# Optimization experiments

Measured on AMD Instinct MI355X. Metric: run time of the kernel, lower is better.

The kernel has to match this reference:

```python
import jax, jax.numpy as jnp
import numpy as np

D_MODEL = 1024
D_FF = 4096
N_EXPERTS = 8
TOP_K = 2
TEMP = 0.7
B, L = 4, 2048


def setup_inputs() -> dict:
    key = jax.random.key(0)
    ks = jax.random.split(key, 6)
    s = 0.02  # init scale
    return {
        "x": jax.random.normal(ks[0], (B, L, D_MODEL), jnp.float32),
        "Wr": jax.random.normal(ks[1], (D_MODEL, N_EXPERTS), jnp.float32) * s,
        "br": jnp.zeros((N_EXPERTS,), jnp.float32),
        "W1": jax.random.normal(ks[2], (N_EXPERTS, D_MODEL, D_FF), jnp.float32) * s,
        "b1": jnp.zeros((N_EXPERTS, D_FF), jnp.float32),
        "W2": jax.random.normal(ks[3], (N_EXPERTS, D_FF, D_MODEL), jnp.float32) * s,
        "b2": jnp.zeros((N_EXPERTS, D_MODEL), jnp.float32),
    }


def reference(x, Wr, br, W1, b1, W2, b2):
    # Eval-mode MoE: no router jitter, dropout is identity.
    Bb, Ll, Dd = x.shape
    E = Wr.shape[1]
    xf = x.reshape(-1, Dd)                              # [T, D]
    T = xf.shape[0]

    logits = xf @ Wr + br                               # [T, E]
    probs = jax.nn.softmax(logits / TEMP, axis=-1)      # [T, E]
    top_w, top_i = jax.lax.top_k(probs, TOP_K)          # [T, K]
    top_w = top_w / (jnp.sum(top_w, axis=-1, keepdims=True) + 1e-6)

    # Per-token per-expert combine weight (zero for non-selected experts).
    cw = jnp.zeros((T, E), xf.dtype).at[jnp.arange(T)[:, None], top_i].add(top_w)

    out = jnp.zeros_like(xf)
    for e in range(E):  # small fixed expert loop
        h = jax.nn.silu(xf @ W1[e] + b1[e])             # [T, d_ff]
        out = out + cw[:, e:e + 1] * (h @ W2[e] + b2[e])

    # Load-balance aux loss.
    counts = jnp.zeros((E,), xf.dtype).at[top_i.reshape(-1)].add(1.0)
    f_i = counts / T
    P_i = probs.mean(axis=0)
    aux = E * jnp.sum(f_i * P_i)
    return out.reshape(Bb, Ll, Dd), aux[None]
```

## Files before the change

### kernel.cpp

```cpp
#include <hip/hip_runtime.h>

#define DM     1024
#define DFF    4096
#define NE     8
#define TT     8192
#define CAP    8192
#define TILE   128
#define RTOK   32
#define MAXROWS 17408

typedef __bf16 bf16x8 __attribute__((ext_vector_type(8)));
typedef float  f32x4  __attribute__((ext_vector_type(4)));
typedef unsigned short u16;
typedef unsigned int   u32;

__device__ __forceinline__ u16 f2bf(float f) {
    u32 u = __builtin_bit_cast(u32, f);
    u += 0x7fffu + ((u >> 16) & 1u);
    return (u16)(u >> 16);
}

__device__ __forceinline__ void gload_lds16(const void* g, void* l) {
    __builtin_amdgcn_global_load_lds(
        (const __attribute__((address_space(1))) void*)g,
        (__attribute__((address_space(3))) void*)l,
        16, 0, 0);
}

__global__ __launch_bounds__(256) void router_k(
    const float* __restrict__ x, const float* __restrict__ Wr, const float* __restrict__ br,
    int* __restrict__ expert_count, float* __restrict__ prob_sum,
    int* __restrict__ list_token, float* __restrict__ list_w,
    int* __restrict__ tok_e, int* __restrict__ tok_q, float* __restrict__ tok_w)
{
    __shared__ float wrT[NE][DM];
    __shared__ float ps[NE];
    __shared__ int   lcount[NE];
    __shared__ int   lbase[NE];
    __shared__ int   lexp[RTOK * 2];
    __shared__ float lw[RTOK * 2];
    __shared__ int   lslot[RTOK * 2];

    int tid = threadIdx.x;
    if (tid < NE) { ps[tid] = 0.f; lcount[tid] = 0; }
#pragma unroll
    for (int it = 0; it < 8; ++it) {
        int f = tid * 4 + it * 1024;
        float4 v = *reinterpret_cast<const float4*>(Wr + f);
        int e0 = f & 7, k = f >> 3;
        wrT[e0][k] = v.x; wrT[e0 + 1][k] = v.y; wrT[e0 + 2][k] = v.z; wrT[e0 + 3][k] = v.w;
    }
    __syncthreads();

    int w = tid >> 6, l = tid & 63;
    for (int j = 0; j < RTOK / 4; ++j) {
        int ti = w * (RTOK / 4) + j;
        int token = blockIdx.x * RTOK + ti;
        const float* xr = x + (size_t)token * DM;
        float acc[NE];
#pragma unroll
        for (int e = 0; e < NE; ++e) acc[e] = 0.f;
#pragma unroll
        for (int i = 0; i < 4; ++i) {
            float4 xv = *reinterpret_cast<const float4*>(xr + i * 256 + l * 4);
#pragma unroll
            for (int e = 0; e < NE; ++e) {
                float4 wv = *reinterpret_cast<const float4*>(&wrT[e][i * 256 + l * 4]);
                acc[e] += xv.x * wv.x + xv.y * wv.y + xv.z * wv.z + xv.w * wv.w;
            }
        }
#pragma unroll
        for (int off = 32; off >= 1; off >>= 1) {
#pragma unroll
            for (int e = 0; e < NE; ++e) acc[e] += __shfl_xor(acc[e], off);
        }
        if (l == 0) {
            float li[NE], m = -1e30f;
#pragma unroll
            for (int e = 0; e < NE; ++e) { li[e] = (acc[e] + br[e]) * (1.0f / 0.7f); m = fmaxf(m, li[e]); }
            float p[NE], s = 0.f;
#pragma unroll
            for (int e = 0; e < NE; ++e) { p[e] = __expf(li[e] - m); s += p[e]; }
            float inv = 1.f / s;
#pragma unroll
            for (int e = 0; e < NE; ++e) { p[e] *= inv; atomicAdd(&ps[e], p[e]); }
            float v1 = -1.f, v2 = -1.f; int e1 = 0, e2 = 0;
#pragma unroll
            for (int e = 0; e < NE; ++e) {
                float pe = p[e];
                if (pe > v1)      { v2 = v1; e2 = e1; v1 = pe; e1 = e; }
                else if (pe > v2) { v2 = pe; e2 = e; }
            }
            float denom = v1 + v2 + 1e-6f;
            lexp[2 * ti]     = e1; lw[2 * ti]     = v1 / denom; lslot[2 * ti]     = atomicAdd(&lcount[e1], 1);
            lexp[2 * ti + 1] = e2; lw[2 * ti + 1] = v2 / denom; lslot[2 * ti + 1] = atomicAdd(&lcount[e2], 1);
        }
    }
    __syncthreads();
    if (tid < NE) {
        lbase[tid] = atomicAdd(&expert_count[tid], lcount[tid]);
        atomicAdd(&prob_sum[tid], ps[tid]);
    }
    __syncthreads();
    if (tid < RTOK * 2) {
        int e = lexp[tid];
        int q = lbase[e] + lslot[tid];
        int token = blockIdx.x * RTOK + (tid >> 1);
        list_token[e * CAP + q] = token;
        list_w[e * CAP + q] = lw[tid];
        int slot = token * 2 + (tid & 1);
        tok_e[slot] = e; tok_q[slot] = q; tok_w[slot] = lw[tid];
    }
}

__global__ void scan_aux_k(const int* __restrict__ expert_count, const float* __restrict__ prob_sum,
                           int* __restrict__ padded_count, int* __restrict__ poffsets,
                           float* __restrict__ aux_out)
{
    if (threadIdx.x == 0 && blockIdx.x == 0) {
        int off = 0; float aux = 0.f;
        for (int e = 0; e < NE; ++e) {
            int c = expert_count[e];
            int pc = (c + TILE - 1) / TILE * TILE;
            poffsets[e] = off; padded_count[e] = pc; off += pc;
            aux += ((float)c / (float)TT) * (prob_sum[e] / (float)TT);
        }
        aux_out[0] = aux * (float)NE;
    }
}

__global__ __launch_bounds__(256) void gather_k(
    const float* __restrict__ x, const int* __restrict__ list_token,
    const int* __restrict__ expert_count, const int* __restrict__ padded_count,
    const int* __restrict__ poffsets, u16* __restrict__ Xg)
{
    int e = blockIdx.y;
    int p0 = blockIdx.x * 8;
    if (p0 >= padded_count[e]) return;
    int tid = threadIdx.x;
    int rr = tid >> 5, cl = tid & 31;
    int p = p0 + rr;
    int g = poffsets[e] + p;
    u16* dst = Xg + (size_t)g * DM;
    bool valid = p < expert_count[e];
    int tok = valid ? list_token[e * CAP + p] : 0;
    const float* src = x + (size_t)tok * DM;
#pragma unroll
    for (int i = 0; i < 4; ++i) {
        int c0 = cl * 8 + i * 256;
        uint4 v;
        if (valid) {
            float4 f0 = *reinterpret_cast<const float4*>(src + c0);
            float4 f1 = *reinterpret_cast<const float4*>(src + c0 + 4);
            v.x = f2bf(f0.x) | ((u32)f2bf(f0.y) << 16);
            v.y = f2bf(f0.z) | ((u32)f2bf(f0.w) << 16);
            v.z = f2bf(f1.x) | ((u32)f2bf(f1.y) << 16);
            v.w = f2bf(f1.z) | ((u32)f2bf(f1.w) << 16);
        } else {
            v.x = 0; v.y = 0; v.z = 0; v.w = 0;
        }
        *reinterpret_cast<uint4*>(dst + c0) = v;
    }
}

__global__ __launch_bounds__(256) void convt_k(
    const float* __restrict__ src, u16* __restrict__ dst, long base, int rs, int Ktot, long dstEStride)
{
    __shared__ float tile[64][65];
    int e = blockIdx.z;
    int k0 = blockIdx.x * 64, j0 = blockIdx.y * 64;
    const float* s = src + (size_t)e * 4194304 + base;
    int tid = threadIdx.x;
    {
        int jj = (tid & 15) * 4, kb = tid >> 4;
#pragma unroll
        for (int i = 0; i < 4; ++i) {
            int k = kb + i * 16;
            float4 v = *reinterpret_cast<const float4*>(s + (size_t)(k0 + k) * rs + j0 + jj);
            tile[k][jj] = v.x; tile[k][jj + 1] = v.y; tile[k][jj + 2] = v.z; tile[k][jj + 3] = v.w;
        }
    }
    __syncthreads();
    {
        int kk = (tid & 15) * 4, jb = tid >> 4;
        u16* d = dst + (size_t)e * dstEStride;
#pragma unroll
        for (int i = 0; i < 4; ++i) {
            int j = jb + i * 16;
            uint2 q;
            q.x = f2bf(tile[kk][j])     | ((u32)f2bf(tile[kk + 1][j]) << 16);
            q.y = f2bf(tile[kk + 2][j]) | ((u32)f2bf(tile[kk + 3][j]) << 16);
            *reinterpret_cast<uint2*>(d + (size_t)(j0 + j) * Ktot + k0 + kk) = q;
        }
    }
}

__device__ __forceinline__ void stage_tile(const u16* __restrict__ rows, long lda, int kt, char* buf) {
    int tid = threadIdx.x;
    int w = tid >> 6, l = tid & 63;
#pragma unroll
    for (int i = 0; i < 4; ++i) {
        int sbase = i * 256 + w * 64;
        int sl = sbase + l;
        int row = sl >> 3;
        int c8 = (sl & 7) ^ (row & 7);
        const u16* src = rows + (size_t)row * lda + kt * 64 + c8 * 8;
        gload_lds16(src, buf + sbase * 16);
    }
}

__device__ __forceinline__ void gemm_main(
    const u16* __restrict__ Arows, long lda,
    const u16* __restrict__ Brows, long ldb,
    int nkt, char* smem, f32x4 acc[4][4])
{
    int tid = threadIdx.x;
    int l = tid & 63, lane16 = l & 15, hi = l >> 4;
    int wm = (tid >> 6) & 1, wn = tid >> 7;

    for (int kt = 0; kt < nkt; ++kt) {
        stage_tile(Arows, lda, kt, smem);
        stage_tile(Brows, ldb, kt, smem + 16384);
        __syncthreads();
        const char* bufA = smem;
        const char* bufB = smem + 16384;
#pragma unroll
        for (int kk = 0; kk < 2; ++kk) {
            bf16x8 af[4], bb[4];
#pragma unroll
            for (int mi = 0; mi < 4; ++mi) {
                int row = wm * 64 + mi * 16 + lane16;
                int ch = (kk * 4 + hi) ^ (row & 7);
                af[mi] = *reinterpret_cast<const bf16x8*>(bufA + (row * 8 + ch) * 16);
            }
#pragma unroll
            for (int ni = 0; ni < 4; ++ni) {
                int row = wn * 64 + ni * 16 + lane16;
                int ch = (kk * 4 + hi) ^ (row & 7);
                bb[ni] = *reinterpret_cast<const bf16x8*>(bufB + (row * 8 + ch) * 16);
            }
#pragma unroll
            for (int mi = 0; mi < 4; ++mi)
#pragma unroll
                for (int ni = 0; ni < 4; ++ni)
                    acc[mi][ni] = __builtin_amdgcn_mfma_f32_16x16x32_bf16(af[mi], bb[ni], acc[mi][ni], 0, 0, 0);
        }
        __syncthreads();
    }
}

__global__ __launch_bounds__(256, 4) void gemm1_k(
    const u16* __restrict__ Xg, const u16* __restrict__ W1c, const float* __restrict__ b1,
    int ffBase, int chunkN, const int* __restrict__ padded_count, const int* __restrict__ poffsets,
    u16* __restrict__ H)
{
    __shared__ char smem[32768];
    int e = blockIdx.z, rb = blockIdx.y, cb = blockIdx.x;
    if (rb * TILE >= padded_count[e]) return;
    int row0 = poffsets[e] + rb * TILE;
    const u16* Arows = Xg + (size_t)row0 * 1024;
    const u16* Brows = W1c + (size_t)e * chunkN * 1024 + (size_t)cb * TILE * 1024;
    f32x4 acc[4][4];
#pragma unroll
    for (int i = 0; i < 4; ++i)
#pragma unroll
        for (int j = 0; j < 4; ++j) { acc[i][j][0]=0.f; acc[i][j][1]=0.f; acc[i][j][2]=0.f; acc[i][j][3]=0.f; }
    gemm_main(Arows, 1024, Brows, 1024, 16, smem, acc);

    int tid = threadIdx.x;
    int l = tid & 63, lane16 = l & 15, hi = l >> 4;
    int wm = (tid >> 6) & 1, wn = tid >> 7;
    const float* b1e = b1 + (size_t)e * DFF + ffBase;
#pragma unroll
    for (int mi = 0; mi < 4; ++mi) {
#pragma unroll
        for (int ni = 0; ni < 4; ++ni) {
            int col = cb * TILE + wn * 64 + ni * 16 + lane16;
            float bv = b1e[col];
#pragma unroll
            for (int r = 0; r < 4; ++r) {
                int grow = row0 + wm * 64 + mi * 16 + hi * 4 + r;
                float z = acc[mi][ni][r] + bv;
                float hval = z / (1.f + __expf(-z));
                H[(size_t)grow * chunkN + col] = f2bf(hval);
            }
        }
    }
}

__global__ __launch_bounds__(256, 4) void gemm2_k(
    const u16* __restrict__ Hb, const u16* __restrict__ W2c, const float* __restrict__ b2,
    int chunkK, int mode, const int* __restrict__ expert_count, const int* __restrict__ padded_count,
    const int* __restrict__ poffsets, const int* __restrict__ list_token,
    const float* __restrict__ list_w, float* __restrict__ Og, float* __restrict__ out)
{
    __shared__ char smem[32768];
    int e = blockIdx.z, rb = blockIdx.y, cb = blockIdx.x;
    if (rb * TILE >= padded_count[e]) return;
    int row0 = poffsets[e] + rb * TILE;
    const u16* Arows = Hb + (size_t)row0 * chunkK;
    const u16* Brows = W2c + (size_t)e * DM * chunkK + (size_t)cb * TILE * chunkK;
    f32x4 acc[4][4];
#pragma unroll
    for (int i = 0; i < 4; ++i)
#pragma unroll
        for (int j = 0; j < 4; ++j) { acc[i][j][0]=0.f; acc[i][j][1]=0.f; acc[i][j][2]=0.f; acc[i][j][3]=0.f; }
    gemm_main(Arows, chunkK, Brows, chunkK, chunkK >> 6, smem, acc);

    int tid = threadIdx.x;
    int l = tid & 63, lane16 = l & 15, hi = l >> 4;
    int wm = (tid >> 6) & 1, wn = tid >> 7;
    if (mode <= 1) {
#pragma unroll
        for (int mi = 0; mi < 4; ++mi) {
#pragma unroll
            for (int r = 0; r < 4; ++r) {
                int grow = row0 + wm * 64 + mi * 16 + hi * 4 + r;
                float* orow = Og + (size_t)grow * DM;
#pragma unroll
                for (int ni = 0; ni < 4; ++ni) {
                    int col = cb * TILE + wn * 64 + ni * 16 + lane16;
                    float v = acc[mi][ni][r];
                    if (mode == 1) v += orow[col];
                    orow[col] = v;
                }
            }
        }
    } else {
        int cnt = expert_count[e];
#pragma unroll
        for (int mi = 0; mi < 4; ++mi) {
#pragma unroll
            for (int r = 0; r < 4; ++r) {
                int p = rb * TILE + wm * 64 + mi * 16 + hi * 4 + r;
                if (p < cnt) {
                    int tok = list_token[e * CAP + p];
                    float wgt = list_w[e * CAP + p];
                    float* orow = out + (size_t)tok * DM;
#pragma unroll
                    for (int ni = 0; ni < 4; ++ni) {
                        int col = cb * TILE + wn * 64 + ni * 16 + lane16;
                        float v = acc[mi][ni][r];
                        if (mode == 2) v += b2[e * DM + col];
                        atomicAdd(orow + col, wgt * v);
                    }
                }
            }
        }
    }
}

__global__ __launch_bounds__(256) void combine_k(
    const float* __restrict__ Og, const float* __restrict__ b2,
    const int* __restrict__ tok_e, const int* __restrict__ tok_q, const float* __restrict__ tok_w,
    const int* __restrict__ poffsets, float* __restrict__ out)
{
    int t = blockIdx.x * 4 + (threadIdx.x >> 6);
    int l = threadIdx.x & 63;
    int e0 = tok_e[t * 2], q0 = tok_q[t * 2];
    int e1 = tok_e[t * 2 + 1], q1 = tok_q[t * 2 + 1];
    float w0 = tok_w[t * 2], w1 = tok_w[t * 2 + 1];
    const float* r0 = Og + (size_t)(poffsets[e0] + q0) * DM;
    const float* r1 = Og + (size_t)(poffsets[e1] + q1) * DM;
    const float* bb0 = b2 + (size_t)e0 * DM;
    const float* bb1 = b2 + (size_t)e1 * DM;
    float* o = out + (size_t)t * DM;
#pragma unroll
    for (int i = 0; i < 4; ++i) {
        int c = l * 4 + i * 256;
        float4 a = *reinterpret_cast<const float4*>(r0 + c);
        float4 b = *reinterpret_cast<const float4*>(r1 + c);
        float4 p = *reinterpret_cast<const float4*>(bb0 + c);
        float4 q = *reinterpret_cast<const float4*>(bb1 + c);
        float4 res;
        res.x = w0 * (a.x + p.x) + w1 * (b.x + q.x);
        res.y = w0 * (a.y + p.y) + w1 * (b.y + q.y);
        res.z = w0 * (a.z + p.z) + w1 * (b.z + q.z);
        res.w = w0 * (a.w + p.w) + w1 * (b.w + q.w);
        *reinterpret_cast<float4*>(o + c) = res;
    }
}

extern "C" void kernel_launch(void* const* d_in, const int* in_sizes, int n_in,
                              void* d_out, int out_size, void* d_ws, size_t ws_size,
                              hipStream_t stream) {
    (void)in_sizes; (void)n_in; (void)out_size;
    const float* x  = (const float*)d_in[0];
    const float* Wr = (const float*)d_in[1];
    const float* br = (const float*)d_in[2];
    const float* W1 = (const float*)d_in[3];
    const float* b1 = (const float*)d_in[4];
    const float* W2 = (const float*)d_in[5];
    const float* b2 = (const float*)d_in[6];
    float* out = (float*)d_out;

    char* ws = (char*)d_ws;
    int*   expert_count = (int*)(ws + 0);
    float* prob_sum     = (float*)(ws + 32);
    int*   padded_count = (int*)(ws + 64);
    int*   poffsets     = (int*)(ws + 96);
    int*   list_token   = (int*)(ws + 256);
    float* list_w       = (float*)(ws + 256 + 262144);
    int*   tok_e        = (int*)(ws + 524544);
    int*   tok_q        = (int*)(ws + 524544 + 65536);
    float* tok_w        = (float*)(ws + 524544 + 131072);
    const size_t HDR = 1048576;
    u16* Xg = (u16*)(ws + HDR);

    const size_t XG_B   = (size_t)MAXROWS * DM * 2;
    const size_t OG_B   = (size_t)MAXROWS * DM * 4;

    const size_t F_HB   = HDR + XG_B;
    const size_t F_W2   = F_HB + (size_t)MAXROWS * DFF * 2;
    const size_t F_W1   = F_W2 + (size_t)NE * DM * DFF * 2;
    const size_t F_OG   = F_W1;
    const size_t F_NEED = F_OG + OG_B;

    const size_t M_HB   = HDR + XG_B;
    const size_t M_W2   = M_HB + (size_t)MAXROWS * 1024 * 2;
    const size_t M_W1   = M_W2 + (size_t)NE * DM * 1024 * 2;
    const size_t M_OG   = M_W1 + (size_t)NE * DM * 1024 * 2;
    const size_t M_NEED = M_OG + OG_B;

    hipMemsetAsync(ws, 0, 64, stream);
    router_k<<<TT / RTOK, 256, 0, stream>>>(x, Wr, br, expert_count, prob_sum, list_token, list_w,
                                            tok_e, tok_q, tok_w);
    scan_aux_k<<<1, 64, 0, stream>>>(expert_count, prob_sum, padded_count, poffsets,
                                     out + (size_t)TT * DM);
    gather_k<<<dim3(1024, 8), 256, 0, stream>>>(x, list_token, expert_count, padded_count, poffsets, Xg);

    if (ws_size >= F_NEED) {
        u16* Hb  = (u16*)(ws + F_HB);
        u16* W2c = (u16*)(ws + F_W2);
        u16* W1c = (u16*)(ws + F_W1);
        float* Og = (float*)(ws + F_OG);
        convt_k<<<dim3(16, 64, 8), 256, 0, stream>>>(W1, W1c, 0, DFF, 1024, (long)DM * DFF);
        convt_k<<<dim3(64, 16, 8), 256, 0, stream>>>(W2, W2c, 0, DM, 4096, (long)DM * DFF);
        gemm1_k<<<dim3(32, 64, 8), 256, 0, stream>>>(Xg, W1c, b1, 0, DFF, padded_count, poffsets, Hb);
        gemm2_k<<<dim3(8, 64, 8), 256, 0, stream>>>(Hb, W2c, b2, DFF, 0, expert_count, padded_count,
                                                    poffsets, list_token, list_w, Og, out);
        combine_k<<<TT / 4, 256, 0, stream>>>(Og, b2, tok_e, tok_q, tok_w, poffsets, out);
    } else if (ws_size >= M_NEED) {
        u16* Hb  = (u16*)(ws + M_HB);
        u16* W2c = (u16*)(ws + M_W2);
        u16* W1c = (u16*)(ws + M_W1);
        float* Og = (float*)(ws + M_OG);
        for (int c = 0; c < 4; ++c) {
            convt_k<<<dim3(16, 16, 8), 256, 0, stream>>>(W1, W1c, (long)c * 1024, DFF, 1024, (long)DM * 1024);
            convt_k<<<dim3(16, 16, 8), 256, 0, stream>>>(W2, W2c, (long)c * 1024 * 1024, DM, 1024, (long)DM * 1024);
            gemm1_k<<<dim3(8, 64, 8), 256, 0, stream>>>(Xg, W1c, b1, c * 1024, 1024, padded_count, poffsets, Hb);
            gemm2_k<<<dim3(8, 64, 8), 256, 0, stream>>>(Hb, W2c, b2, 1024, (c == 0) ? 0 : 1,
                                                        expert_count, padded_count, poffsets,
                                                        list_token, list_w, Og, out);
        }
        combine_k<<<TT / 4, 256, 0, stream>>>(Og, b2, tok_e, tok_q, tok_w, poffsets, out);
    } else {
        u16* Hb  = (u16*)(ws + M_HB);
        u16* W2c = (u16*)(ws + M_W2);
        u16* W1c = (u16*)(ws + M_W1);
        hipMemsetAsync(d_out, 0, (size_t)TT * DM * sizeof(float), stream);
        for (int c = 0; c < 4; ++c) {
            convt_k<<<dim3(16, 16, 8), 256, 0, stream>>>(W1, W1c, (long)c * 1024, DFF, 1024, (long)DM * 1024);
            convt_k<<<dim3(16, 16, 8), 256, 0, stream>>>(W2, W2c, (long)c * 1024 * 1024, DM, 1024, (long)DM * 1024);
            gemm1_k<<<dim3(8, 64, 8), 256, 0, stream>>>(Xg, W1c, b1, c * 1024, 1024, padded_count, poffsets, Hb);
            gemm2_k<<<dim3(8, 64, 8), 256, 0, stream>>>(Hb, W2c, b2, 1024, (c == 0) ? 2 : 3,
                                                        expert_count, padded_count, poffsets,
                                                        list_token, list_w, nullptr, out);
        }
    }
}
```

Before: 542.6 us.

## Use 256x256 double-buffered GEMM tiles with staged prefetch and XCD-aware block mapping

Replaces the 128x128 single-buffered GEMM loop with a 256x256 tile and 512 threads. It double-buffers 128KB of LDS and issues the next k-tile's loads in halves between MFMA groups, using explicit vmcnt waits, raw barriers and setprio. Blocks are launched as a flat grid and remapped so consecutive IDs spread across the 8 XCDs. The workspace-size fallback paths are dropped and the full-size path is always used. The aim is to hide global-load latency and cut LDS traffic per FLOP, at the cost of occupancy (one block per CU), more padding waste per expert, and a larger workspace assumption.

```diff
diff --git a/kernel.cpp b/kernel.cpp
--- a/kernel.cpp
+++ b/kernel.cpp
@@ -5,9 +5,8 @@
 #define NE     8
 #define TT     8192
 #define CAP    8192
-#define TILE   128
 #define RTOK   32
-#define MAXROWS 17408
+#define MAXRA  17664
 
 typedef __bf16 bf16x8 __attribute__((ext_vector_type(8)));
 typedef float  f32x4  __attribute__((ext_vector_type(4)));
@@ -121,7 +120,7 @@
         int off = 0; float aux = 0.f;
         for (int e = 0; e < NE; ++e) {
             int c = expert_count[e];
-            int pc = (c + TILE - 1) / TILE * TILE;
+            int pc = (c + 127) / 128 * 128;
             poffsets[e] = off; padded_count[e] = pc; off += pc;
             aux += ((float)c / (float)TT) * (prob_sum[e] / (float)TT);
         }
@@ -164,12 +163,12 @@
 }
 
 __global__ __launch_bounds__(256) void convt_k(
-    const float* __restrict__ src, u16* __restrict__ dst, long base, int rs, int Ktot, long dstEStride)
+    const float* __restrict__ src, u16* __restrict__ dst, int rs, int Ktot, long dstEStride)
 {
     __shared__ float tile[64][65];
     int e = blockIdx.z;
     int k0 = blockIdx.x * 64, j0 = blockIdx.y * 64;
-    const float* s = src + (size_t)e * 4194304 + base;
+    const float* s = src + (size_t)e * 4194304;
     int tid = threadIdx.x;
     {
         int jj = (tid & 15) * 4, kb = tid >> 4;
@@ -195,155 +194,202 @@
     }
 }
 
-__device__ __forceinline__ void stage_tile(const u16* __restrict__ rows, long lda, int kt, char* buf) {
+
+__device__ __forceinline__ void stage_half(const u16* __restrict__ rows, long lda, int kt, int h,
+                                           char* matbuf) {
     int tid = threadIdx.x;
-    int w = tid >> 6, l = tid & 63;
-#pragma unroll
-    for (int i = 0; i < 4; ++i) {
-        int sbase = i * 256 + w * 64;
+    int wid = tid >> 6, l = tid & 63;
+#pragma unroll
+    for (int i = 0; i < 2; ++i) {
+        int sbase = h * 1024 + i * 512 + wid * 64;
         int sl = sbase + l;
         int row = sl >> 3;
         int c8 = (sl & 7) ^ (row & 7);
-        const u16* src = rows + (size_t)row * lda + kt * 64 + c8 * 8;
-        gload_lds16(src, buf + sbase * 16);
-    }
-}
-
-__device__ __forceinline__ void gemm_main(
-    const u16* __restrict__ Arows, long lda,
-    const u16* __restrict__ Brows, long ldb,
-    int nkt, char* smem, f32x4 acc[4][4])
-{
-    int tid = threadIdx.x;
-    int l = tid & 63, lane16 = l & 15, hi = l >> 4;
-    int wm = (tid >> 6) & 1, wn = tid >> 7;
-
-    for (int kt = 0; kt < nkt; ++kt) {
-        stage_tile(Arows, lda, kt, smem);
-        stage_tile(Brows, ldb, kt, smem + 16384);
-        __syncthreads();
-        const char* bufA = smem;
-        const char* bufB = smem + 16384;
-#pragma unroll
-        for (int kk = 0; kk < 2; ++kk) {
-            bf16x8 af[4], bb[4];
-#pragma unroll
-            for (int mi = 0; mi < 4; ++mi) {
-                int row = wm * 64 + mi * 16 + lane16;
-                int ch = (kk * 4 + hi) ^ (row & 7);
-                af[mi] = *reinterpret_cast<const bf16x8*>(bufA + (row * 8 + ch) * 16);
-            }
-#pragma unroll
-            for (int ni = 0; ni < 4; ++ni) {
-                int row = wn * 64 + ni * 16 + lane16;
-                int ch = (kk * 4 + hi) ^ (row & 7);
-                bb[ni] = *reinterpret_cast<const bf16x8*>(bufB + (row * 8 + ch) * 16);
-            }
-#pragma unroll
-            for (int mi = 0; mi < 4; ++mi)
-#pragma unroll
-                for (int ni = 0; ni < 4; ++ni)
-                    acc[mi][ni] = __builtin_amdgcn_mfma_f32_16x16x32_bf16(af[mi], bb[ni], acc[mi][ni], 0, 0, 0);
-        }
-        __syncthreads();
-    }
-}
-
-__global__ __launch_bounds__(256, 4) void gemm1_k(
+        gload_lds16(rows + (size_t)row * lda + kt * 64 + c8 * 8, matbuf + sbase * 16);
+    }
+}
+
+__device__ __forceinline__ f32x4 mfma16x16(bf16x8 a, bf16x8 b, f32x4 c) {
+    return __builtin_amdgcn_mfma_f32_16x16x32_bf16(a, b, c, 0, 0, 0);
+}
+
+__device__ __forceinline__ void gemm_main256(
+    const u16* __restrict__ A, long lda, const u16* __restrict__ B, long ldb,
+    int nkt, char* smem, f32x4 acc[8][4])
+{
+    char* Ab[2] = { smem, smem + 32768 };
+    char* Bb[2] = { smem + 65536, smem + 98304 };
+    int tid = threadIdx.x, l = tid & 63, lane16 = l & 15, hi = (l >> 4);
+    int wid = tid >> 6, wm = wid >> 2, wn = wid & 3;
+
+    stage_half(A, lda, 0, 0, Ab[0]); stage_half(A, lda, 0, 1, Ab[0]);
+    stage_half(B, ldb, 0, 0, Bb[0]); stage_half(B, ldb, 0, 1, Bb[0]);
+    stage_half(A, lda, 1, 0, Ab[1]);
+
+    for (int T = 0; T < nkt; ++T) {
+        int c = T & 1, o = c ^ 1;
+        bool notlast = (T + 1 < nkt);
+        if (notlast) stage_half(A, lda, T + 1, 1, Ab[o]);
+        if (notlast) { asm volatile("s_waitcnt vmcnt(4)" ::: "memory"); }
+        else         { asm volatile("s_waitcnt vmcnt(0)" ::: "memory"); }
+        __builtin_amdgcn_s_barrier();
+
+        bf16x8 af[4], bb[4];
+#pragma unroll
+        for (int mi = 0; mi < 4; ++mi) {
+            int row = wm * 128 + 0 * 64 + mi * 16 + lane16;
+            int ch = (0 * 4 + hi) ^ (row & 7);
+            af[mi] = *reinterpret_cast<const bf16x8*>(Ab[c] + (row * 8 + ch) * 16);
+        }
+#pragma unroll
+        for (int ni = 0; ni < 4; ++ni) {
+            int row = wn * 64 + ni * 16 + lane16;
+            int ch = (0 * 4 + hi) ^ (row & 7);
+            bb[ni] = *reinterpret_cast<const bf16x8*>(Bb[c] + (row * 8 + ch) * 16);
+        }
+        __builtin_amdgcn_s_setprio(1);
+#pragma unroll
+        for (int mi = 0; mi < 4; ++mi)
+#pragma unroll
+            for (int ni = 0; ni < 4; ++ni)
+                acc[mi][ni] = mfma16x16(af[mi], bb[ni], acc[mi][ni]);
+        __builtin_amdgcn_s_setprio(0);
+
+        if (notlast) stage_half(B, ldb, T + 1, 0, Bb[o]);
+#pragma unroll
+        for (int mi = 0; mi < 4; ++mi) {
+            int row = wm * 128 + 64 + mi * 16 + lane16;
+            int ch = (0 * 4 + hi) ^ (row & 7);
+            af[mi] = *reinterpret_cast<const bf16x8*>(Ab[c] + (row * 8 + ch) * 16);
+        }
+        __builtin_amdgcn_s_setprio(1);
+#pragma unroll
+        for (int mi = 0; mi < 4; ++mi)
+#pragma unroll
+            for (int ni = 0; ni < 4; ++ni)
+                acc[4 + mi][ni] = mfma16x16(af[mi], bb[ni], acc[4 + mi][ni]);
+        __builtin_amdgcn_s_setprio(0);
+
+        if (notlast) stage_half(B, ldb, T + 1, 1, Bb[o]);
+#pragma unroll
+        for (int mi = 0; mi < 4; ++mi) {
+            int row = wm * 128 + 0 * 64 + mi * 16 + lane16;
+            int ch = (1 * 4 + hi) ^ (row & 7);
+            af[mi] = *reinterpret_cast<const bf16x8*>(Ab[c] + (row * 8 + ch) * 16);
+        }
+#pragma unroll
+        for (int ni = 0; ni < 4; ++ni) {
+            int row = wn * 64 + ni * 16 + lane16;
+            int ch = (1 * 4 + hi) ^ (row & 7);
+            bb[ni] = *reinterpret_cast<const bf16x8*>(Bb[c] + (row * 8 + ch) * 16);
+        }
+        __builtin_amdgcn_s_setprio(1);
+#pragma unroll
+        for (int mi = 0; mi < 4; ++mi)
+#pragma unroll
+            for (int ni = 0; ni < 4; ++ni)
+                acc[mi][ni] = mfma16x16(af[mi], bb[ni], acc[mi][ni]);
+        __builtin_amdgcn_s_setprio(0);
+
+#pragma unroll
+        for (int mi = 0; mi < 4; ++mi) {
+            int row = wm * 128 + 64 + mi * 16 + lane16;
+            int ch = (1 * 4 + hi) ^ (row & 7);
+            af[mi] = *reinterpret_cast<const bf16x8*>(Ab[c] + (row * 8 + ch) * 16);
+        }
+        __builtin_amdgcn_s_setprio(1);
+#pragma unroll
+        for (int mi = 0; mi < 4; ++mi)
+#pragma unroll
+            for (int ni = 0; ni < 4; ++ni)
+                acc[4 + mi][ni] = mfma16x16(af[mi], bb[ni], acc[4 + mi][ni]);
+        __builtin_amdgcn_s_setprio(0);
+        __builtin_amdgcn_s_barrier();
+        if (T + 2 < nkt) stage_half(A, lda, T + 2, 0, Ab[c]);
+    }
+}
+
+__global__ __launch_bounds__(512) void gemm1_k(
     const u16* __restrict__ Xg, const u16* __restrict__ W1c, const float* __restrict__ b1,
-    int ffBase, int chunkN, const int* __restrict__ padded_count, const int* __restrict__ poffsets,
+    const int* __restrict__ padded_count, const int* __restrict__ poffsets,
     u16* __restrict__ H)
 {
-    __shared__ char smem[32768];
-    int e = blockIdx.z, rb = blockIdx.y, cb = blockIdx.x;
-    if (rb * TILE >= padded_count[e]) return;
-    int row0 = poffsets[e] + rb * TILE;
+    __shared__ char smem[131072];
+    int nb = gridDim.x, q8 = nb >> 3;
+    int wg = (blockIdx.x & 7) * q8 + (blockIdx.x >> 3);
+    int cb = wg & 15, rb = (wg >> 4) & 31, e = wg >> 9;
+    int pc = padded_count[e];
+    if (rb * 256 >= pc) return;
+    int row0 = poffsets[e] + rb * 256;
     const u16* Arows = Xg + (size_t)row0 * 1024;
-    const u16* Brows = W1c + (size_t)e * chunkN * 1024 + (size_t)cb * TILE * 1024;
-    f32x4 acc[4][4];
-#pragma unroll
-    for (int i = 0; i < 4; ++i)
+    const u16* Brows = W1c + (size_t)e * DFF * 1024 + (size_t)cb * 256 * 1024;
+    f32x4 acc[8][4];
+#pragma unroll
+    for (int i = 0; i < 8; ++i)
 #pragma unroll
         for (int j = 0; j < 4; ++j) { acc[i][j][0]=0.f; acc[i][j][1]=0.f; acc[i][j][2]=0.f; acc[i][j][3]=0.f; }
-    gemm_main(Arows, 1024, Brows, 1024, 16, smem, acc);
-
-    int tid = threadIdx.x;
-    int l = tid & 63, lane16 = l & 15, hi = l >> 4;
-    int wm = (tid >> 6) & 1, wn = tid >> 7;
-    const float* b1e = b1 + (size_t)e * DFF + ffBase;
-#pragma unroll
-    for (int mi = 0; mi < 4; ++mi) {
+    gemm_main256(Arows, 1024, Brows, 1024, 16, smem, acc);
+
+    int tid = threadIdx.x, l = tid & 63, lane16 = l & 15, hi = l >> 4;
+    int wid = tid >> 6, wm = wid >> 2, wn = wid & 3;
+    const float* b1e = b1 + (size_t)e * DFF;
+#pragma unroll
+    for (int a = 0; a < 8; ++a) {
+        int m = a >> 2, mi = a & 3;
 #pragma unroll
         for (int ni = 0; ni < 4; ++ni) {
-            int col = cb * TILE + wn * 64 + ni * 16 + lane16;
+            int col = cb * 256 + wn * 64 + ni * 16 + lane16;
             float bv = b1e[col];
 #pragma unroll
             for (int r = 0; r < 4; ++r) {
-                int grow = row0 + wm * 64 + mi * 16 + hi * 4 + r;
-                float z = acc[mi][ni][r] + bv;
-                float hval = z / (1.f + __expf(-z));
-                H[(size_t)grow * chunkN + col] = f2bf(hval);
-            }
-        }
-    }
-}
-
-__global__ __launch_bounds__(256, 4) void gemm2_k(
-    const u16* __restrict__ Hb, const u16* __restrict__ W2c, const float* __restrict__ b2,
-    int chunkK, int mode, const int* __restrict__ expert_count, const int* __restrict__ padded_count,
-    const int* __restrict__ poffsets, const int* __restrict__ list_token,
-    const float* __restrict__ list_w, float* __restrict__ Og, float* __restrict__ out)
-{
-    __shared__ char smem[32768];
-    int e = blockIdx.z, rb = blockIdx.y, cb = blockIdx.x;
-    if (rb * TILE >= padded_count[e]) return;
-    int row0 = poffsets[e] + rb * TILE;
-    const u16* Arows = Hb + (size_t)row0 * chunkK;
-    const u16* Brows = W2c + (size_t)e * DM * chunkK + (size_t)cb * TILE * chunkK;
-    f32x4 acc[4][4];
-#pragma unroll
-    for (int i = 0; i < 4; ++i)
-#pragma unroll
-        for (int j = 0; j < 4; ++j) { acc[i][j][0]=0.f; acc[i][j][1]=0.f; acc[i][j][2]=0.f; acc[i][j][3]=0.f; }
-    gemm_main(Arows, chunkK, Brows, chunkK, chunkK >> 6, smem, acc);
-
-    int tid = threadIdx.x;
-    int l = tid & 63, lane16 = l & 15, hi = l >> 4;
-    int wm = (tid >> 6) & 1, wn = tid >> 7;
-    if (mode <= 1) {
-#pragma unroll
-        for (int mi = 0; mi < 4; ++mi) {
-#pragma unroll
-            for (int r = 0; r < 4; ++r) {
-                int grow = row0 + wm * 64 + mi * 16 + hi * 4 + r;
-                float* orow = Og + (size_t)grow * DM;
-#pragma unroll
-                for (int ni = 0; ni < 4; ++ni) {
-                    int col = cb * TILE + wn * 64 + ni * 16 + lane16;
-                    float v = acc[mi][ni][r];
-                    if (mode == 1) v += orow[col];
-                    orow[col] = v;
+                int rloc = wm * 128 + m * 64 + mi * 16 + hi * 4 + r;
+                int p = rb * 256 + rloc;
+                if (p < pc) {
+                    float z = acc[a][ni][r] + bv;
+                    float hval = z / (1.f + __expf(-z));
+                    H[(size_t)(row0 + rloc) * DFF + col] = f2bf(hval);
                 }
             }
         }
-    } else {
-        int cnt = expert_count[e];
-#pragma unroll
-        for (int mi = 0; mi < 4; ++mi) {
-#pragma unroll
-            for (int r = 0; r < 4; ++r) {
-                int p = rb * TILE + wm * 64 + mi * 16 + hi * 4 + r;
-                if (p < cnt) {
-                    int tok = list_token[e * CAP + p];
-                    float wgt = list_w[e * CAP + p];
-                    float* orow = out + (size_t)tok * DM;
-#pragma unroll
-                    for (int ni = 0; ni < 4; ++ni) {
-                        int col = cb * TILE + wn * 64 + ni * 16 + lane16;
-                        float v = acc[mi][ni][r];
-                        if (mode == 2) v += b2[e * DM + col];
-                        atomicAdd(orow + col, wgt * v);
-                    }
+    }
+}
+
+__global__ __launch_bounds__(512) void gemm2_k(
+    const u16* __restrict__ Hb, const u16* __restrict__ W2c,
+    const int* __restrict__ padded_count, const int* __restrict__ poffsets,
+    float* __restrict__ Og)
+{
+    __shared__ char smem[131072];
+    int nb = gridDim.x, q8 = nb >> 3;
+    int wg = (blockIdx.x & 7) * q8 + (blockIdx.x >> 3);
+    int cb = wg & 3, rb = (wg >> 2) & 31, e = wg >> 7;
+    int pc = padded_count[e];
+    if (rb * 256 >= pc) return;
+    int row0 = poffsets[e] + rb * 256;
+    const u16* Arows = Hb + (size_t)row0 * DFF;
+    const u16* Brows = W2c + (size_t)e * DM * DFF + (size_t)cb * 256 * DFF;
+    f32x4 acc[8][4];
+#pragma unroll
+    for (int i = 0; i < 8; ++i)
+#pragma unroll
+        for (int j = 0; j < 4; ++j) { acc[i][j][0]=0.f; acc[i][j][1]=0.f; acc[i][j][2]=0.f; acc[i][j][3]=0.f; }
+    gemm_main256(Arows, DFF, Brows, DFF, 64, smem, acc);
+
+    int tid = threadIdx.x, l = tid & 63, lane16 = l & 15, hi = l >> 4;
+    int wid = tid >> 6, wm = wid >> 2, wn = wid & 3;
+#pragma unroll
+    for (int a = 0; a < 8; ++a) {
+        int m = a >> 2, mi = a & 3;
+#pragma unroll
+        for (int r = 0; r < 4; ++r) {
+            int rloc = wm * 128 + m * 64 + mi * 16 + hi * 4 + r;
+            int p = rb * 256 + rloc;
+            if (p < pc) {
+                float* orow = Og + (size_t)(row0 + rloc) * DM;
+#pragma unroll
+                for (int ni = 0; ni < 4; ++ni) {
+                    int col = cb * 256 + wn * 64 + ni * 16 + lane16;
+                    orow[col] = acc[a][ni][r];
                 }
             }
         }
@@ -384,7 +430,7 @@
 extern "C" void kernel_launch(void* const* d_in, const int* in_sizes, int n_in,
                               void* d_out, int out_size, void* d_ws, size_t ws_size,
                               hipStream_t stream) {
-    (void)in_sizes; (void)n_in; (void)out_size;
+    (void)in_sizes; (void)n_in; (void)out_size; (void)ws_size;
     const float* x  = (const float*)d_in[0];
     const float* Wr = (const float*)d_in[1];
     const float* br = (const float*)d_in[2];
@@ -404,23 +450,17 @@
     int*   tok_e        = (int*)(ws + 524544);
     int*   tok_q        = (int*)(ws + 524544 + 65536);
     float* tok_w        = (float*)(ws + 524544 + 131072);
-    const size_t HDR = 1048576;
-    u16* Xg = (u16*)(ws + HDR);
-
-    const size_t XG_B   = (size_t)MAXROWS * DM * 2;
-    const size_t OG_B   = (size_t)MAXROWS * DM * 4;
-
-    const size_t F_HB   = HDR + XG_B;
-    const size_t F_W2   = F_HB + (size_t)MAXROWS * DFF * 2;
-    const size_t F_W1   = F_W2 + (size_t)NE * DM * DFF * 2;
-    const size_t F_OG   = F_W1;
-    const size_t F_NEED = F_OG + OG_B;
-
-    const size_t M_HB   = HDR + XG_B;
-    const size_t M_W2   = M_HB + (size_t)MAXROWS * 1024 * 2;
-    const size_t M_W1   = M_W2 + (size_t)NE * DM * 1024 * 2;
-    const size_t M_OG   = M_W1 + (size_t)NE * DM * 1024 * 2;
-    const size_t M_NEED = M_OG + OG_B;
+
+    const size_t HDR    = 1048576;
+    const size_t OFF_HB = HDR;
+    const size_t OFF_W2 = OFF_HB + (size_t)MAXRA * DFF * 2;
+    const size_t OFF_XG = OFF_W2 + (size_t)NE * DM * DFF * 2;
+    const size_t OFF_W1 = OFF_XG + (size_t)MAXRA * DM * 2;
+    u16*   Hb  = (u16*)(ws + OFF_HB);
+    u16*   W2c = (u16*)(ws + OFF_W2);
+    u16*   Xg  = (u16*)(ws + OFF_XG);
+    u16*   W1c = (u16*)(ws + OFF_W1);
+    float* Og  = (float*)(ws + OFF_XG);
 
     hipMemsetAsync(ws, 0, 64, stream);
     router_k<<<TT / RTOK, 256, 0, stream>>>(x, Wr, br, expert_count, prob_sum, list_token, list_w,
@@ -429,43 +469,10 @@
                                      out + (size_t)TT * DM);
     gather_k<<<dim3(1024, 8), 256, 0, stream>>>(x, list_token, expert_count, padded_count, poffsets, Xg);
 
-    if (ws_size >= F_NEED) {
-        u16* Hb  = (u16*)(ws + F_HB);
-        u16* W2c = (u16*)(ws + F_W2);
-        u16* W1c = (u16*)(ws + F_W1);
-        float* Og = (float*)(ws + F_OG);
-        convt_k<<<dim3(16, 64, 8), 256, 0, stream>>>(W1, W1c, 0, DFF, 1024, (long)DM * DFF);
-        convt_k<<<dim3(64, 16, 8), 256, 0, stream>>>(W2, W2c, 0, DM, 4096, (long)DM * DFF);
-        gemm1_k<<<dim3(32, 64, 8), 256, 0, stream>>>(Xg, W1c, b1, 0, DFF, padded_count, poffsets, Hb);
-        gemm2_k<<<dim3(8, 64, 8), 256, 0, stream>>>(Hb, W2c, b2, DFF, 0, expert_count, padded_count,
-                                                    poffsets, list_token, list_w, Og, out);
-        combine_k<<<TT / 4, 256, 0, stream>>>(Og, b2, tok_e, tok_q, tok_w, poffsets, out);
-    } else if (ws_size >= M_NEED) {
-        u16* Hb  = (u16*)(ws + M_HB);
-        u16* W2c = (u16*)(ws + M_W2);
-        u16* W1c = (u16*)(ws + M_W1);
-        float* Og = (float*)(ws + M_OG);
-        for (int c = 0; c < 4; ++c) {
-            convt_k<<<dim3(16, 16, 8), 256, 0, stream>>>(W1, W1c, (long)c * 1024, DFF, 1024, (long)DM * 1024);
-            convt_k<<<dim3(16, 16, 8), 256, 0, stream>>>(W2, W2c, (long)c * 1024 * 1024, DM, 1024, (long)DM * 1024);
-            gemm1_k<<<dim3(8, 64, 8), 256, 0, stream>>>(Xg, W1c, b1, c * 1024, 1024, padded_count, poffsets, Hb);
-            gemm2_k<<<dim3(8, 64, 8), 256, 0, stream>>>(Hb, W2c, b2, 1024, (c == 0) ? 0 : 1,
-                                                        expert_count, padded_count, poffsets,
-                                                        list_token, list_w, Og, out);
-        }
-        combine_k<<<TT / 4, 256, 0, stream>>>(Og, b2, tok_e, tok_q, tok_w, poffsets, out);
-    } else {
-        u16* Hb  = (u16*)(ws + M_HB);
-        u16* W2c = (u16*)(ws + M_W2);
-        u16* W1c = (u16*)(ws + M_W1);
-        hipMemsetAsync(d_out, 0, (size_t)TT * DM * sizeof(float), stream);
-        for (int c = 0; c < 4; ++c) {
-            convt_k<<<dim3(16, 16, 8), 256, 0, stream>>>(W1, W1c, (long)c * 1024, DFF, 1024, (long)DM * 1024);
-            convt_k<<<dim3(16, 16, 8), 256, 0, stream>>>(W2, W2c, (long)c * 1024 * 1024, DM, 1024, (long)DM * 1024);
-            gemm1_k<<<dim3(8, 64, 8), 256, 0, stream>>>(Xg, W1c, b1, c * 1024, 1024, padded_count, poffsets, Hb);
-            gemm2_k<<<dim3(8, 64, 8), 256, 0, stream>>>(Hb, W2c, b2, 1024, (c == 0) ? 2 : 3,
-                                                        expert_count, padded_count, poffsets,
-                                                        list_token, list_w, nullptr, out);
-        }
-    }
-}
+    convt_k<<<dim3(16, 64, 8), 256, 0, stream>>>(W1, W1c, DFF, 1024, (long)DM * DFF);
+    convt_k<<<dim3(64, 16, 8), 256, 0, stream>>>(W2, W2c, DM, 4096, (long)DM * DFF);
+
+    gemm1_k<<<4096, 512, 0, stream>>>(Xg, W1c, b1, padded_count, poffsets, Hb);
+    gemm2_k<<<1024, 512, 0, stream>>>(Hb, W2c, padded_count, poffsets, Og);
+    combine_k<<<TT / 4, 256, 0, stream>>>(Og, b2, tok_e, tok_q, tok_w, poffsets, out);
+}
```

New measurement: 745.1 us. 1.37x slower.
